# Kernel tuning notes

Measured on AMD Instinct MI355X. Metric: run time of the kernel, lower is better.

## Reference

```python
import jax, jax.numpy as jnp
import numpy as np
import math

B, D, S, H = 4, 1024, 2048, 16


def setup_inputs() -> dict:
    key = jax.random.key(0)
    ks = jax.random.split(key, 9)
    scale = 0.02
    return {
        "x": jax.random.normal(ks[0], (B, D, S), dtype=jnp.float32),
        "Wq": jax.random.normal(ks[1], (D, D), dtype=jnp.float32) * scale,
        "bq": jnp.zeros((D,), dtype=jnp.float32),
        "Wk": jax.random.normal(ks[2], (D, D), dtype=jnp.float32) * scale,
        "bk": jnp.zeros((D,), dtype=jnp.float32),
        "Wv": jax.random.normal(ks[3], (D, D), dtype=jnp.float32) * scale,
        "bv": jnp.zeros((D,), dtype=jnp.float32),
        "Wo": jax.random.normal(ks[4], (D, D), dtype=jnp.float32) * scale,
        "bo": jnp.zeros((D,), dtype=jnp.float32),
        "num_heads": H,
    }


def _positional_encoding(d_model, seq_len):
    # pe[0::2, :] = sin(pos * denom), pe[1::2, :] = cos(pos * denom)
    pos = jnp.arange(seq_len, dtype=jnp.float32)[None, :]            # [1, S]
    denom = jnp.exp(jnp.arange(0, d_model, 2, dtype=jnp.float32)
                    * (-math.log(10000.0) / d_model))[:, None]        # [D/2, 1]
    angles = pos * denom                                              # [D/2, S]
    pe = jnp.zeros((d_model, seq_len), dtype=jnp.float32)
    pe = pe.at[0::2, :].set(jnp.sin(angles))
    pe = pe.at[1::2, :].set(jnp.cos(angles))
    return pe


def reference(x, Wq, bq, Wk, bk, Wv, bv, Wo, bo, num_heads):
    b, d_model, s = x.shape
    head_dim = d_model // num_heads
    x = x + _positional_encoding(d_model, s)[None, :, :]  # broadcast over batch
    x = jnp.transpose(x, (0, 2, 1))                       # [B, S, D]
    q = x @ Wq.T + bq
    k = x @ Wk.T + bk
    v = x @ Wv.T + bv
    # [B, S, H, hd] -> [B, H, S, hd]
    q = q.reshape(b, s, num_heads, head_dim).transpose(0, 2, 1, 3)
    k = k.reshape(b, s, num_heads, head_dim).transpose(0, 2, 1, 3)
    v = v.reshape(b, s, num_heads, head_dim).transpose(0, 2, 1, 3)
    scores = jnp.einsum('bhqd,bhkd->bhqk', q, k) / jnp.sqrt(
        jnp.asarray(head_dim, dtype=jnp.float32))
    attn = jax.nn.softmax(scores, axis=-1)
    out = jnp.einsum('bhqk,bhkd->bhqd', attn, v)          # [B, H, S, hd]
    out = out.transpose(0, 2, 1, 3).reshape(b, s, d_model)
    out = out @ Wo.T + bo
    return jnp.transpose(out, (0, 2, 1))                  # [B, D, S]
```

## Files before the change

kernel.cpp:

```cpp
#include <hip/hip_runtime.h>


typedef __bf16 bf16;
typedef __attribute__((ext_vector_type(8))) __bf16 bf16x8;
typedef __attribute__((ext_vector_type(4))) __bf16 bf16x4;
typedef __attribute__((ext_vector_type(4))) float f32x4;

#define NB 4
#define ND 1024
#define NS 2048
#define NH 16
#define NM 8192

__device__ __forceinline__ void gld16(const void* g, void* l) {
  __builtin_amdgcn_global_load_lds((__attribute__((address_space(1))) void*)g,
                                   (__attribute__((address_space(3))) void*)l, 16, 0, 0);
}

__device__ __forceinline__ int swz4(int r) { return (r + (r >> 2)) & 3; }

__global__ __launch_bounds__(256) void prep_x_kernel(const float* __restrict__ x,
                                                     bf16* __restrict__ xT) {
  __shared__ float t[32][33];
  const int tx = threadIdx.x, ty = threadIdx.y;
  const int s0 = blockIdx.x * 32, d0 = blockIdx.y * 32, b = blockIdx.z;
#pragma unroll
  for (int i = 0; i < 4; ++i) {
    const int rr = ty + i * 8;
    const int d = d0 + rr, s = s0 + tx;
    const float freq = __expf(-(float)(d >> 1) * 0.01798894603980689f);
    const float ang = (float)s * freq;
    const float pe = (d & 1) ? cosf(ang) : sinf(ang);
    t[rr][tx] = x[((size_t)b * ND + d) * NS + s] + pe;
  }
  __syncthreads();
#pragma unroll
  for (int i = 0; i < 4; ++i) {
    const int a = ty + i * 8;
    xT[((size_t)b * NS + s0 + a) * ND + d0 + tx] = (bf16)t[tx][a];
  }
}

__global__ __launch_bounds__(256) void prep_w_kernel(const float* __restrict__ Wq,
                                                     const float* __restrict__ Wk,
                                                     const float* __restrict__ Wv,
                                                     const float* __restrict__ Wo,
                                                     bf16* __restrict__ Wqkv,
                                                     bf16* __restrict__ WoB) {
  const size_t t = (size_t)blockIdx.x * blockDim.x + threadIdx.x;
  const size_t i = t * 4;
  const float* src;
  bf16* dst;
  size_t off;
  if (i < (size_t)3 * 1024 * 1024) {
    const int sel = (int)(i >> 20);
    src = sel == 0 ? Wq : (sel == 1 ? Wk : Wv);
    off = i - ((size_t)sel << 20);
    dst = Wqkv + i;
  } else {
    src = Wo;
    off = i - ((size_t)3 << 20);
    dst = WoB + off;
  }
  const f32x4 v = *(const f32x4*)(src + off);
  bf16x4 o;
  o[0] = (bf16)v[0];
  o[1] = (bf16)v[1];
  o[2] = (bf16)v[2];
  o[3] = (bf16)v[3];
  *(bf16x4*)dst = o;
}

__device__ __forceinline__ void gemm_tile_128(const bf16* __restrict__ A,
                                              const bf16* __restrict__ Bm,
                                              int tm, int tn, bf16* ldsA, bf16* ldsB,
                                              f32x4 acc[4][4]) {
  const int tid = threadIdx.x;
  const int lane = tid & 63, wave = tid >> 6;
  const int wm = wave >> 1, wn = wave & 1;
  const int rl = lane & 15, quad = lane >> 4;
  const int sw = swz4(rl);
  int r0[2], c0[2], ld0[2];
#pragma unroll
  for (int j = 0; j < 2; ++j) {
    const int chunk = wave * 2 + j;
    const int o = chunk * 1024 + lane * 16;
    const int r = o >> 6;
    r0[j] = r;
    c0[j] = (((o >> 4) & 3) ^ swz4(r)) * 8;
    ld0[j] = chunk * 1024;
  }
  for (int kt = 0; kt < 1024; kt += 32) {
#pragma unroll
    for (int j = 0; j < 2; ++j) {
      gld16(A + (size_t)(tm + r0[j]) * 1024 + kt + c0[j], (char*)ldsA + ld0[j]);
      gld16(Bm + (size_t)(tn + r0[j]) * 1024 + kt + c0[j], (char*)ldsB + ld0[j]);
    }
    __syncthreads();
    bf16x8 af[4], bfr[4];
#pragma unroll
    for (int i = 0; i < 4; ++i) {
      const int ra = wm * 64 + i * 16 + rl;
      af[i] = *(const bf16x8*)((const char*)ldsA + ra * 64 + ((quad ^ sw) * 16));
      const int rb = wn * 64 + i * 16 + rl;
      bfr[i] = *(const bf16x8*)((const char*)ldsB + rb * 64 + ((quad ^ sw) * 16));
    }
#pragma unroll
    for (int i = 0; i < 4; ++i)
#pragma unroll
      for (int j = 0; j < 4; ++j)
        acc[i][j] = __builtin_amdgcn_mfma_f32_16x16x32_bf16(af[i], bfr[j], acc[i][j], 0, 0, 0);
    __syncthreads();
  }
}

__global__ __launch_bounds__(256, 2) void gemm_qkv_kernel(
    const bf16* __restrict__ xT, const bf16* __restrict__ Wqkv,
    const float* __restrict__ bq, const float* __restrict__ bk,
    const float* __restrict__ bv, bf16* __restrict__ Q, bf16* __restrict__ Kb,
    bf16* __restrict__ VT) {
  __shared__ bf16 ldsA[128 * 32], ldsB[128 * 32];
  const int tm = blockIdx.x * 128, tn = blockIdx.y * 128;
  f32x4 acc[4][4];
  const f32x4 z = {0.f, 0.f, 0.f, 0.f};
#pragma unroll
  for (int i = 0; i < 4; ++i)
#pragma unroll
    for (int j = 0; j < 4; ++j) acc[i][j] = z;
  gemm_tile_128(xT, Wqkv, tm, tn, ldsA, ldsB, acc);
  const int lane = threadIdx.x & 63, wave = threadIdx.x >> 6;
  const int wm = wave >> 1, wn = wave & 1;
  const int rl = lane & 15, quad = lane >> 4;
#pragma unroll
  for (int j = 0; j < 4; ++j) {
    const int n = tn + wn * 64 + j * 16 + rl;
    const int which = n >> 10;
    const int nl = n & 1023;
    const int h = nl >> 6, d = nl & 63;
    const float bias = (which == 0 ? bq : which == 1 ? bk : bv)[nl];
#pragma unroll
    for (int i = 0; i < 4; ++i) {
      const int m0 = tm + wm * 64 + i * 16 + quad * 4;
      const int b = m0 >> 11, s0 = m0 & 2047;
      const size_t bh = (size_t)(b * 16 + h);
      if (which == 2) {
        bf16x4 pk;
#pragma unroll
        for (int r = 0; r < 4; ++r) pk[r] = (bf16)(acc[i][j][r] + bias);
        *(bf16x4*)(VT + ((size_t)bh * 64 + d) * 2048 + s0) = pk;
      } else {
#pragma unroll
        for (int r = 0; r < 4; ++r) {
          const float v = acc[i][j][r] + bias;
          const int s = s0 + r;
          if (which == 0)
            Q[(bh * 2048 + s) * 64 + d] = (bf16)(v * 0.125f);
          else
            Kb[(bh * 2048 + s) * 64 + d] = (bf16)v;
        }
      }
    }
  }
}

__global__ __launch_bounds__(256, 3) void attn_kernel(const bf16* __restrict__ Q,
                                                      const bf16* __restrict__ Kb,
                                                      const bf16* __restrict__ VT,
                                                      bf16* __restrict__ AO) {
  __shared__ __align__(16) char smem[51200];
  char* ldsK = smem;
  char* ldsV = smem + 16384;
  char* ldsPQ = smem + 32768;
  const int tid = threadIdx.x;
  const int lane = tid & 63, wave = tid >> 6;
  const int rl = lane & 15, quad = lane >> 4;
  const int bh = blockIdx.y;
  const int q0 = blockIdx.x * 128;
  const bf16* Qb = Q + ((size_t)bh * 2048 + q0) * 64;
  const bf16* Kbb = Kb + (size_t)bh * 2048 * 64;
  const bf16* Vb = VT + (size_t)bh * 64 * 2048;
  for (int ch = wave; ch < 16; ch += 4) {
    const int o = ch * 1024 + lane * 16;
    const int r = o >> 7;
    const int c = (((o >> 4) & 7) ^ (r & 7)) * 16;
    gld16((const char*)Qb + (size_t)r * 128 + c, ldsPQ + ch * 1024);
  }
  {
    const int o0 = wave * 1024 + lane * 16, o1 = o0 + 4096;
    const int ra = o0 >> 7, rb = o1 >> 7;
    const int ca = (((o0 >> 4) & 7) ^ (ra & 7)) * 16;
    const int cb = (((o1 >> 4) & 7) ^ (rb & 7)) * 16;
    gld16((const char*)Kbb + (size_t)ra * 128 + ca, ldsK + wave * 1024);
    gld16((const char*)Kbb + (size_t)rb * 128 + cb, ldsK + wave * 1024 + 4096);
    gld16((const char*)Vb + (size_t)ra * 4096 + ca, ldsV + wave * 1024);
    gld16((const char*)Vb + (size_t)rb * 4096 + cb, ldsV + wave * 1024 + 4096);
  }
  __syncthreads();
  bf16x8 qf[2][2];
#pragma unroll
  for (int i = 0; i < 2; ++i)
#pragma unroll
    for (int ks = 0; ks < 2; ++ks) {
      const int row = wave * 32 + i * 16 + rl;
      qf[i][ks] = *(const bf16x8*)(ldsPQ + row * 128 + (((ks * 4 + quad) ^ (rl & 7)) * 16));
    }
  f32x4 o_acc[2][4];
  float l_part[2];
  const f32x4 z = {0.f, 0.f, 0.f, 0.f};
#pragma unroll
  for (int i = 0; i < 2; ++i) {
    l_part[i] = 0.f;
#pragma unroll
    for (int j = 0; j < 4; ++j) o_acc[i][j] = z;
  }
  int buf = 0;
  for (int kt = 0; kt < 2048; kt += 64, buf ^= 1) {
    __syncthreads();
    if (kt + 64 < 2048) {
      const int nb = (buf ^ 1) * 8192;
      const int o0 = wave * 1024 + lane * 16, o1 = o0 + 4096;
      const int ra = o0 >> 7, rb = o1 >> 7;
      const int ca = (((o0 >> 4) & 7) ^ (ra & 7)) * 16;
      const int cb = (((o1 >> 4) & 7) ^ (rb & 7)) * 16;
      gld16((const char*)Kbb + (size_t)(kt + 64 + ra) * 128 + ca, ldsK + nb + wave * 1024);
      gld16((const char*)Kbb + (size_t)(kt + 64 + rb) * 128 + cb,
            ldsK + nb + wave * 1024 + 4096);
      gld16((const char*)Vb + (size_t)ra * 4096 + (size_t)(kt + 64) * 2 + ca,
            ldsV + nb + wave * 1024);
      gld16((const char*)Vb + (size_t)rb * 4096 + (size_t)(kt + 64) * 2 + cb,
            ldsV + nb + wave * 1024 + 4096);
    }
    f32x4 sacc[4][2];
#pragma unroll
    for (int j = 0; j < 4; ++j)
#pragma unroll
      for (int i = 0; i < 2; ++i) sacc[j][i] = z;
#pragma unroll
    for (int ks = 0; ks < 2; ++ks) {
#pragma unroll
      for (int j = 0; j < 4; ++j) {
        const bf16x8 kf = *(const bf16x8*)(ldsK + buf * 8192 + (j * 16 + rl) * 128 +
                                           (((ks * 4 + quad) ^ (rl & 7)) * 16));
#pragma unroll
        for (int i = 0; i < 2; ++i)
          sacc[j][i] =
              __builtin_amdgcn_mfma_f32_16x16x32_bf16(kf, qf[i][ks], sacc[j][i], 0, 0, 0);
      }
    }
#pragma unroll
    for (int i = 0; i < 2; ++i)
#pragma unroll
      for (int j = 0; j < 4; ++j) {
        bf16x4 pk;
#pragma unroll
        for (int r = 0; r < 4; ++r) {
          const float p = __expf(sacc[j][i][r]);
          l_part[i] += p;
          pk[r] = (bf16)p;
        }
        *(bf16x4*)(ldsPQ + (wave * 32 + i * 16 + rl) * 144 + (j * 16 + quad * 4) * 2) = pk;
      }
    asm volatile("s_waitcnt lgkmcnt(0)\n\ts_barrier" ::: "memory");
#pragma unroll
    for (int ks = 0; ks < 2; ++ks) {
      bf16x8 pf[2];
#pragma unroll
      for (int i = 0; i < 2; ++i)
        pf[i] = *(const bf16x8*)(ldsPQ + (wave * 32 + i * 16 + rl) * 144 + ks * 64 +
                                 quad * 16);
#pragma unroll
      for (int j = 0; j < 4; ++j) {
        const bf16x8 vf = *(const bf16x8*)(ldsV + buf * 8192 + (j * 16 + rl) * 128 +
                                           (((ks * 4 + quad) ^ (rl & 7)) * 16));
#pragma unroll
        for (int i = 0; i < 2; ++i)
          o_acc[i][j] =
              __builtin_amdgcn_mfma_f32_16x16x32_bf16(pf[i], vf, o_acc[i][j], 0, 0, 0);
      }
    }
  }
  __syncthreads();
  float* ldsL = (float*)smem;
#pragma unroll
  for (int i = 0; i < 2; ++i) {
    float l = l_part[i];
    l += __shfl_xor(l, 16);
    l += __shfl_xor(l, 32);
    if (quad == 0) ldsL[wave * 32 + i * 16 + rl] = 1.f / l;
  }
  __syncthreads();
  const int b = bh >> 4, h = bh & 15;
#pragma unroll
  for (int i = 0; i < 2; ++i) {
    const f32x4 linv = *(const f32x4*)(ldsL + wave * 32 + i * 16 + quad * 4);
#pragma unroll
    for (int j = 0; j < 4; ++j)
#pragma unroll
      for (int r = 0; r < 4; ++r) {
        const int s = q0 + wave * 32 + i * 16 + quad * 4 + r;
        const int d = h * 64 + j * 16 + rl;
        AO[((size_t)b * 2048 + s) * 1024 + d] = (bf16)(o_acc[i][j][r] * linv[r]);
      }
  }
}

__global__ __launch_bounds__(256, 2) void gemm_out_kernel(const bf16* __restrict__ AO,
                                                          const bf16* __restrict__ WoB,
                                                          const float* __restrict__ bo,
                                                          float* __restrict__ out) {
  __shared__ bf16 ldsA[128 * 32], ldsB[128 * 32];
  const int tm = blockIdx.x * 128, tn = blockIdx.y * 128;
  f32x4 acc[4][4];
  const f32x4 z = {0.f, 0.f, 0.f, 0.f};
#pragma unroll
  for (int i = 0; i < 4; ++i)
#pragma unroll
    for (int j = 0; j < 4; ++j) acc[i][j] = z;
  gemm_tile_128(AO, WoB, tm, tn, ldsA, ldsB, acc);
  const int lane = threadIdx.x & 63, wave = threadIdx.x >> 6;
  const int wm = wave >> 1, wn = wave & 1;
  const int rl = lane & 15, quad = lane >> 4;
#pragma unroll
  for (int j = 0; j < 4; ++j) {
    const int n = tn + wn * 64 + j * 16 + rl;
    const float bias = bo[n];
#pragma unroll
    for (int i = 0; i < 4; ++i) {
      const int m0 = tm + wm * 64 + i * 16 + quad * 4;
      const int b = m0 >> 11, s = m0 & 2047;
      f32x4 v = acc[i][j];
      v[0] += bias;
      v[1] += bias;
      v[2] += bias;
      v[3] += bias;
      *(f32x4*)(out + ((size_t)(b * 1024 + n)) * 2048 + s) = v;
    }
  }
}

extern "C" void kernel_launch(void* const* d_in, const int* in_sizes, int n_in,
                              void* d_out, int out_size, void* d_ws, size_t ws_size,
                              hipStream_t stream) {
  const float* x = (const float*)d_in[0];
  const float* Wq = (const float*)d_in[1];
  const float* bq = (const float*)d_in[2];
  const float* Wk = (const float*)d_in[3];
  const float* bk = (const float*)d_in[4];
  const float* Wv = (const float*)d_in[5];
  const float* bv = (const float*)d_in[6];
  const float* Wo = (const float*)d_in[7];
  const float* bo = (const float*)d_in[8];
  float* out = (float*)d_out;

  char* p = (char*)d_ws;
  bf16* xT = (bf16*)p;
  p += (size_t)NM * ND * 2;
  bf16* Wqkv = (bf16*)p;
  p += (size_t)3 * ND * ND * 2;
  bf16* WoB = (bf16*)p;
  p += (size_t)ND * ND * 2;
  bf16* Qb = (bf16*)p;
  p += (size_t)NM * ND * 2;
  bf16* Kbf = (bf16*)p;
  p += (size_t)NM * ND * 2;
  bf16* VTb = (bf16*)p;
  p += (size_t)NM * ND * 2;
  bf16* AO = xT;

  prep_x_kernel<<<dim3(NS / 32, ND / 32, NB), dim3(32, 8), 0, stream>>>(x, xT);
  prep_w_kernel<<<dim3(4096), dim3(256), 0, stream>>>(Wq, Wk, Wv, Wo, Wqkv, WoB);
  gemm_qkv_kernel<<<dim3(NM / 128, 3072 / 128), dim3(256), 0, stream>>>(
      xT, Wqkv, bq, bk, bv, Qb, Kbf, VTb);
  attn_kernel<<<dim3(NS / 128, NB * NH), dim3(256), 0, stream>>>(Qb, Kbf, VTb, AO);
  gemm_out_kernel<<<dim3(NM / 128, ND / 128), dim3(256), 0, stream>>>(AO, WoB, bo, out);
}
```

Measured before the change: 303.3 us.

## Use exp2 softmax, MFMA row sums, per-wave P buffer, and swapped attention grid

Folds log2(e) into the Q scale so the attention kernel can use the hardware exp2 instead of __expf. Row sums come from an extra MFMA against a ones vector, which removes the per-element scalar adds, the cross-lane shuffles and the LDS round trip at the end. Each wave now writes P to its own swizzled LDS region, so the block-wide barrier between the P write and the P read is dropped, and LDS shrinks slightly. The grid dimensions are swapped so consecutive blocks cover different heads rather than different query tiles of the same head, which changes L2 locality for K/V. Skipping max subtraction still relies on small scores, and the row sum now adds the bf16-rounded P values rather than the fp32 ones.

```diff
diff --git a/kernel.cpp b/kernel.cpp
--- a/kernel.cpp
+++ b/kernel.cpp
@@ -18,6 +18,14 @@
 }
 
 __device__ __forceinline__ int swz4(int r) { return (r + (r >> 2)) & 3; }
+
+__device__ __forceinline__ float exp2_fast(float x) {
+#if __has_builtin(__builtin_amdgcn_exp2f)
+  return __builtin_amdgcn_exp2f(x);
+#else
+  return exp2f(x);
+#endif
+}
 
 __global__ __launch_bounds__(256) void prep_x_kernel(const float* __restrict__ x,
                                                      bf16* __restrict__ xT) {
@@ -131,6 +139,7 @@
   const int lane = threadIdx.x & 63, wave = threadIdx.x >> 6;
   const int wm = wave >> 1, wn = wave & 1;
   const int rl = lane & 15, quad = lane >> 4;
+  const float QSCALE = 0.18033688011112042f;
 #pragma unroll
   for (int j = 0; j < 4; ++j) {
     const int n = tn + wn * 64 + j * 16 + rl;
@@ -154,7 +163,7 @@
           const float v = acc[i][j][r] + bias;
           const int s = s0 + r;
           if (which == 0)
-            Q[(bh * 2048 + s) * 64 + d] = (bf16)(v * 0.125f);
+            Q[(bh * 2048 + s) * 64 + d] = (bf16)(v * QSCALE);
           else
             Kb[(bh * 2048 + s) * 64 + d] = (bf16)v;
         }
@@ -167,15 +176,15 @@
                                                       const bf16* __restrict__ Kb,
                                                       const bf16* __restrict__ VT,
                                                       bf16* __restrict__ AO) {
-  __shared__ __align__(16) char smem[51200];
+  __shared__ __align__(16) char smem[49152];
   char* ldsK = smem;
   char* ldsV = smem + 16384;
   char* ldsPQ = smem + 32768;
   const int tid = threadIdx.x;
   const int lane = tid & 63, wave = tid >> 6;
   const int rl = lane & 15, quad = lane >> 4;
-  const int bh = blockIdx.y;
-  const int q0 = blockIdx.x * 128;
+  const int bh = blockIdx.x;
+  const int q0 = blockIdx.y * 128;
   const bf16* Qb = Q + ((size_t)bh * 2048 + q0) * 64;
   const bf16* Kbb = Kb + (size_t)bh * 2048 * 64;
   const bf16* Vb = VT + (size_t)bh * 64 * 2048;
@@ -185,16 +194,14 @@
     const int c = (((o >> 4) & 7) ^ (r & 7)) * 16;
     gld16((const char*)Qb + (size_t)r * 128 + c, ldsPQ + ch * 1024);
   }
-  {
-    const int o0 = wave * 1024 + lane * 16, o1 = o0 + 4096;
-    const int ra = o0 >> 7, rb = o1 >> 7;
-    const int ca = (((o0 >> 4) & 7) ^ (ra & 7)) * 16;
-    const int cb = (((o1 >> 4) & 7) ^ (rb & 7)) * 16;
-    gld16((const char*)Kbb + (size_t)ra * 128 + ca, ldsK + wave * 1024);
-    gld16((const char*)Kbb + (size_t)rb * 128 + cb, ldsK + wave * 1024 + 4096);
-    gld16((const char*)Vb + (size_t)ra * 4096 + ca, ldsV + wave * 1024);
-    gld16((const char*)Vb + (size_t)rb * 4096 + cb, ldsV + wave * 1024 + 4096);
-  }
+  const int o0 = wave * 1024 + lane * 16, o1 = o0 + 4096;
+  const int ra = o0 >> 7, rb = o1 >> 7;
+  const int ca = (((o0 >> 4) & 7) ^ (ra & 7)) * 16;
+  const int cb = (((o1 >> 4) & 7) ^ (rb & 7)) * 16;
+  gld16((const char*)Kbb + (size_t)ra * 128 + ca, ldsK + wave * 1024);
+  gld16((const char*)Kbb + (size_t)rb * 128 + cb, ldsK + wave * 1024 + 4096);
+  gld16((const char*)Vb + (size_t)ra * 4096 + ca, ldsV + wave * 1024);
+  gld16((const char*)Vb + (size_t)rb * 4096 + cb, ldsV + wave * 1024 + 4096);
   __syncthreads();
   bf16x8 qf[2][2];
 #pragma unroll
@@ -204,24 +211,22 @@
       const int row = wave * 32 + i * 16 + rl;
       qf[i][ks] = *(const bf16x8*)(ldsPQ + row * 128 + (((ks * 4 + quad) ^ (rl & 7)) * 16));
     }
-  f32x4 o_acc[2][4];
-  float l_part[2];
+  f32x4 o_acc[2][4], lacc[2];
   const f32x4 z = {0.f, 0.f, 0.f, 0.f};
 #pragma unroll
   for (int i = 0; i < 2; ++i) {
-    l_part[i] = 0.f;
+    lacc[i] = z;
 #pragma unroll
     for (int j = 0; j < 4; ++j) o_acc[i][j] = z;
   }
+  const bf16 oneb = (bf16)1.0f;
+  const bf16x8 onesb = {oneb, oneb, oneb, oneb, oneb, oneb, oneb, oneb};
+  char* Pw = ldsPQ + wave * 4096;
   int buf = 0;
   for (int kt = 0; kt < 2048; kt += 64, buf ^= 1) {
     __syncthreads();
     if (kt + 64 < 2048) {
       const int nb = (buf ^ 1) * 8192;
-      const int o0 = wave * 1024 + lane * 16, o1 = o0 + 4096;
-      const int ra = o0 >> 7, rb = o1 >> 7;
-      const int ca = (((o0 >> 4) & 7) ^ (ra & 7)) * 16;
-      const int cb = (((o1 >> 4) & 7) ^ (rb & 7)) * 16;
       gld16((const char*)Kbb + (size_t)(kt + 64 + ra) * 128 + ca, ldsK + nb + wave * 1024);
       gld16((const char*)Kbb + (size_t)(kt + 64 + rb) * 128 + cb,
             ldsK + nb + wave * 1024 + 4096);
@@ -253,21 +258,20 @@
       for (int j = 0; j < 4; ++j) {
         bf16x4 pk;
 #pragma unroll
-        for (int r = 0; r < 4; ++r) {
-          const float p = __expf(sacc[j][i][r]);
-          l_part[i] += p;
-          pk[r] = (bf16)p;
-        }
-        *(bf16x4*)(ldsPQ + (wave * 32 + i * 16 + rl) * 144 + (j * 16 + quad * 4) * 2) = pk;
-      }
-    asm volatile("s_waitcnt lgkmcnt(0)\n\ts_barrier" ::: "memory");
+        for (int r = 0; r < 4; ++r) pk[r] = (bf16)exp2_fast(sacc[j][i][r]);
+        *(bf16x4*)(Pw + (i * 2 + (j >> 1)) * 1024 + rl * 64 +
+                   ((((j & 1) * 2 + (quad >> 1)) ^ (rl & 3)) * 16) + (quad & 1) * 8) = pk;
+      }
+    asm volatile("s_waitcnt lgkmcnt(0)" ::: "memory");
 #pragma unroll
     for (int ks = 0; ks < 2; ++ks) {
       bf16x8 pf[2];
 #pragma unroll
       for (int i = 0; i < 2; ++i)
-        pf[i] = *(const bf16x8*)(ldsPQ + (wave * 32 + i * 16 + rl) * 144 + ks * 64 +
-                                 quad * 16);
+        pf[i] = *(const bf16x8*)(Pw + (i * 2 + ks) * 1024 + rl * 64 +
+                                 ((quad ^ (rl & 3)) * 16));
+      lacc[0] = __builtin_amdgcn_mfma_f32_16x16x32_bf16(pf[0], onesb, lacc[0], 0, 0, 0);
+      lacc[1] = __builtin_amdgcn_mfma_f32_16x16x32_bf16(pf[1], onesb, lacc[1], 0, 0, 0);
 #pragma unroll
       for (int j = 0; j < 4; ++j) {
         const bf16x8 vf = *(const bf16x8*)(ldsV + buf * 8192 + (j * 16 + rl) * 128 +
@@ -279,20 +283,12 @@
       }
     }
   }
-  __syncthreads();
-  float* ldsL = (float*)smem;
+  const int b = bh >> 4, h = bh & 15;
 #pragma unroll
   for (int i = 0; i < 2; ++i) {
-    float l = l_part[i];
-    l += __shfl_xor(l, 16);
-    l += __shfl_xor(l, 32);
-    if (quad == 0) ldsL[wave * 32 + i * 16 + rl] = 1.f / l;
-  }
-  __syncthreads();
-  const int b = bh >> 4, h = bh & 15;
-#pragma unroll
-  for (int i = 0; i < 2; ++i) {
-    const f32x4 linv = *(const f32x4*)(ldsL + wave * 32 + i * 16 + quad * 4);
+    f32x4 linv;
+#pragma unroll
+    for (int r = 0; r < 4; ++r) linv[r] = __builtin_amdgcn_rcpf(lacc[i][r]);
 #pragma unroll
     for (int j = 0; j < 4; ++j)
 #pragma unroll
@@ -371,6 +367,6 @@
   prep_w_kernel<<<dim3(4096), dim3(256), 0, stream>>>(Wq, Wk, Wv, Wo, Wqkv, WoB);
   gemm_qkv_kernel<<<dim3(NM / 128, 3072 / 128), dim3(256), 0, stream>>>(
       xT, Wqkv, bq, bk, bv, Qb, Kbf, VTb);
-  attn_kernel<<<dim3(NS / 128, NB * NH), dim3(256), 0, stream>>>(Qb, Kbf, VTb, AO);
+  attn_kernel<<<dim3(NB * NH, NS / 128), dim3(256), 0, stream>>>(Qb, Kbf, VTb, AO);
   gemm_out_kernel<<<dim3(NM / 128, ND / 128), dim3(256), 0, stream>>>(AO, WoB, bo, out);
 }
```

Result: no change. 299.8 us (-1.2%).
